# Kernel tuning notes

Measured on AMD Instinct MI355X. Metric: run time of the kernel, lower is better.

Reference implementation:

```python
import jax, jax.numpy as jnp
import numpy as np

T, B, I, H, O, L = 256, 128, 128, 512, 1, 5


def setup_inputs() -> dict:
    key = jax.random.key(0)
    ks = jax.random.split(key, 12)
    k = 1.0 / np.sqrt(H)
    u = lambda kk, shape: jax.random.uniform(kk, shape, jnp.float32, -k, k)
    inp = {
        "input_seq": jax.random.normal(ks[0], (T, B, I), jnp.float32),
        # layer 0: input size I, 2 directions
        "W_ih0": u(ks[1], (2, 3 * H, I)),
        "W_hh0": u(ks[2], (2, 3 * H, H)),
        "b_ih0": u(ks[3], (2, 3 * H)),
        "b_hh0": u(ks[4], (2, 3 * H)),
        # layers 1..4: input size 2H, 2 directions
        "W_ih": u(ks[5], (L - 1, 2, 3 * H, 2 * H)),
        "W_hh": u(ks[6], (L - 1, 2, 3 * H, H)),
        "b_ih": u(ks[7], (L - 1, 2, 3 * H)),
        "b_hh": u(ks[8], (L - 1, 2, 3 * H)),
        "fc_w": u(ks[9], (O, 2 * H)),
        "fc_b": u(ks[10], (O,)),
    }
    return inp


def _gru_dir(x, Wih, Whh, bih, bhh):
    # x: [T, B, in]; precompute input-side gates for all timesteps
    gx = jnp.einsum('tbi,gi->tbg', x, Wih) + bih  # [T, B, 3H]

    def step(h, g):
        gh = h @ Whh.T + bhh  # [B, 3H]
        xr, xz, xn = jnp.split(g, 3, axis=-1)
        hr, hz, hn = jnp.split(gh, 3, axis=-1)
        r = jax.nn.sigmoid(xr + hr)
        z = jax.nn.sigmoid(xz + hz)
        n = jnp.tanh(xn + r * hn)
        h_new = (1.0 - z) * n + z * h
        return h_new, h_new

    h0 = jnp.zeros((x.shape[1], Whh.shape[1]), x.dtype)
    _, hs = jax.lax.scan(step, h0, gx)
    return hs  # [T, B, H]


def _bigru_layer(x, Wih, Whh, bih, bhh):
    # Wih: [2, 3H, in]; direction 0 = forward, 1 = backward (PyTorch convention)
    fwd = _gru_dir(x, Wih[0], Whh[0], bih[0], bhh[0])
    bwd = _gru_dir(x[::-1], Wih[1], Whh[1], bih[1], bhh[1])[::-1]
    return jnp.concatenate([fwd, bwd], axis=-1)  # [T, B, 2H]


def reference(input_seq, W_ih0, W_hh0, b_ih0, b_hh0, W_ih, W_hh, b_ih, b_hh, fc_w, fc_b):
    # 5-layer bidirectional GRU (eval mode: inter-layer dropout inactive)
    h = _bigru_layer(input_seq, W_ih0, W_hh0, b_ih0, b_hh0)
    for l in range(L - 1):
        h = _bigru_layer(h, W_ih[l], W_hh[l], b_ih[l], b_hh[l])
    out = jnp.einsum('tbh,oh->tbo', h, fc_w) + fc_b
    return jax.nn.sigmoid(out)
```

## Files before the change

### kernel.cpp

```cpp
#include <hip/hip_runtime.h>
#include <hip/hip_bf16.h>

#define T_ 256
#define B_ 128
#define H_ 512
#define G3 1536
#define SCH 32
#define NCH 8
#define RWG 32
#define BGRP 8

typedef __attribute__((ext_vector_type(8))) short short8;
typedef __attribute__((ext_vector_type(4))) short short4v;
typedef __attribute__((ext_vector_type(4))) float f32x4;

static __device__ __forceinline__ float b2f(short s){
    unsigned u = ((unsigned)(unsigned short)s) << 16;
    return __builtin_bit_cast(float, u);
}
static __device__ __forceinline__ short f2b(float f){
    __hip_bfloat16 h = __float2bfloat16(f);
    return __builtin_bit_cast(short, h);
}
static __device__ __forceinline__ void gload16(const void* g, void* l){
    __builtin_amdgcn_global_load_lds(
        (__attribute__((address_space(1))) void*)(void*)g,
        (__attribute__((address_space(3))) void*)l, 16, 0, 0);
}
static __device__ __forceinline__ short8 gload_sc(const short* p){
    short8 v;
    asm volatile("global_load_dwordx4 %0, %1, off sc0 sc1"
                 : "=v"(v) : "v"(p) : "memory");
    return v;
}
static __device__ __forceinline__ void gstore_sc(short* p, short v){
    asm volatile("global_store_short %0, %1, off sc0 sc1"
                 :: "v"(p), "v"(v) : "memory");
}
static __device__ __forceinline__ void wait_vm0(){
    asm volatile("s_waitcnt vmcnt(0)" ::: "memory");
}

__global__ void cvt_f32_to_bf16(const float* __restrict__ src, short* __restrict__ dst, int n){
    int i = (blockIdx.x * blockDim.x + threadIdx.x) * 4;
    int stride = gridDim.x * blockDim.x * 4;
    for (; i + 3 < n; i += stride){
        float4 v = *(const float4*)(src + i);
        short4v o;
        o[0] = f2b(v.x); o[1] = f2b(v.y); o[2] = f2b(v.z); o[3] = f2b(v.w);
        *(short4v*)(dst + i) = o;
    }
}

__global__ __launch_bounds__(256) void gx_gemm(
    const short* __restrict__ A,
    const short* __restrict__ W,
    const float* __restrict__ bias,
    short* __restrict__ gxc,
    int K, int t0f, int t0b_lo)
{
    __shared__ __align__(16) short sA[4096];
    __shared__ __align__(16) short sB[4096];
    const int dir = blockIdx.z;
    const int t0 = dir ? t0b_lo : t0f;
    const int m0 = blockIdx.x * 128;
    const int n0 = blockIdx.y * 128;
    const short* Ae = A + (size_t)(t0 * B_) * K;
    const short* We = W + (size_t)dir * G3 * K;
    short* out = gxc + (size_t)dir * ((size_t)SCH * B_ * G3);

    const int tid = threadIdx.x, wv = tid >> 6, lane = tid & 63;
    const int moff = (wv & 1) * 64, noff = (wv >> 1) * 64;
    const int e0 = wv * 1024 + lane * 8, e1 = e0 + 512;
    const short* a0 = Ae + (size_t)(m0 + (e0 >> 5)) * K + (e0 & 31);
    const short* a1 = Ae + (size_t)(m0 + (e1 >> 5)) * K + (e1 & 31);
    const short* b0 = We + (size_t)(n0 + (e0 >> 5)) * K + (e0 & 31);
    const short* b1 = We + (size_t)(n0 + (e1 >> 5)) * K + (e1 & 31);
    short* sa0 = &sA[wv * 1024];  short* sa1 = &sA[wv * 1024 + 512];
    short* sb0 = &sB[wv * 1024];  short* sb1 = &sB[wv * 1024 + 512];

    f32x4 acc[4][4] = {};
    const int lr = lane & 15, lk = (lane >> 4) * 8;

    for (int kk = 0; kk < K; kk += 32){
        gload16(a0 + kk, sa0); gload16(a1 + kk, sa1);
        gload16(b0 + kk, sb0); gload16(b1 + kk, sb1);
        __syncthreads();
        short8 ar[4], br[4];
        #pragma unroll
        for (int i = 0; i < 4; ++i) ar[i] = *(const short8*)&sA[(moff + i*16 + lr) * 32 + lk];
        #pragma unroll
        for (int i = 0; i < 4; ++i) br[i] = *(const short8*)&sB[(noff + i*16 + lr) * 32 + lk];
        #pragma unroll
        for (int ai = 0; ai < 4; ++ai)
            #pragma unroll
            for (int bi = 0; bi < 4; ++bi)
                acc[ai][bi] = __builtin_amdgcn_mfma_f32_16x16x32_bf16(ar[ai], br[bi], acc[ai][bi], 0, 0, 0);
        __syncthreads();
    }

    #pragma unroll
    for (int ai = 0; ai < 4; ++ai){
        #pragma unroll
        for (int bi = 0; bi < 4; ++bi){
            int col = n0 + noff + bi*16 + lr;
            float bv = bias[dir * G3 + col];
            #pragma unroll
            for (int r = 0; r < 4; ++r){
                int row = m0 + moff + ai*16 + ((lane >> 4) << 2) + r;
                out[(size_t)row * G3 + col] = f2b(acc[ai][bi][r] + bv);
            }
        }
    }
}

__global__ __launch_bounds__(256, 1) void rec_kernel(
    const short* __restrict__ gxc,
    const short* __restrict__ Whh,
    const float* __restrict__ bhh,
    short* __restrict__ xout,
    float* __restrict__ hfm,
    short* __restrict__ hbb,
    int* __restrict__ bar,
    int t0f, int t0b_hi, int first, int base)
{
    __shared__ __align__(16) short lds_h[32 * 520];
    const int tid = threadIdx.x, wv = tid >> 6, lane = tid & 63;
    const int ug = blockIdx.x >> 2, bg = blockIdx.x & 3, dir = blockIdx.y;
    const int u0 = ug * 64 + wv * 16;
    const int m0 = bg * 32;
    const int lr = lane & 15, lk = (lane >> 4) * 8;
    const int crow = (lane >> 4) * 4;

    const short* Wd = Whh + (size_t)dir * G3 * H_;
    short8 wreg[3][16];
    #pragma unroll
    for (int g = 0; g < 3; ++g)
        #pragma unroll
        for (int kk = 0; kk < 16; ++kk)
            wreg[g][kk] = *(const short8*)&Wd[(size_t)(g*H_ + u0 + lr) * H_ + kk*32 + lk];

    float bh[3];
    #pragma unroll
    for (int g = 0; g < 3; ++g) bh[g] = bhh[dir*G3 + g*H_ + u0 + lr];

    float hreg[2][4];
    #pragma unroll
    for (int mt = 0; mt < 2; ++mt)
        #pragma unroll
        for (int r = 0; r < 4; ++r)
            hreg[mt][r] = first ? 0.f
                : hfm[((size_t)dir*B_ + m0 + mt*16 + crow + r)*H_ + u0 + lr];

    int* cnt = bar + (dir*4 + bg) * 32;
    const short* gxd = gxc + (size_t)dir * ((size_t)SCH * B_ * G3);

    const int srow = tid >> 3, scol0 = (tid & 7) * 8;

    float gv[3][2][4];
    {
        const int tl0 = dir ? (SCH - 1) : 0;
        const short* gb = gxd + ((size_t)(tl0 * B_) + m0 + crow) * G3 + u0 + lr;
        #pragma unroll
        for (int g = 0; g < 3; ++g)
            #pragma unroll
            for (int mt = 0; mt < 2; ++mt)
                #pragma unroll
                for (int r = 0; r < 4; ++r)
                    gv[g][mt][r] = b2f(gb[(size_t)(mt*16 + r) * G3 + g * H_]);
    }

    for (int sl = 0; sl < SCH; ++sl){
        const int t  = dir ? (t0b_hi - sl) : (t0f + sl);
        const int rp = sl & 1;

        {
            const short* hsrc = hbb + ((size_t)(rp*2 + dir) * B_ + m0) * H_;
            short8 hv[8];
            #pragma unroll
            for (int c = 0; c < 8; ++c)
                hv[c] = gload_sc(hsrc + (size_t)srow * H_ + scol0 + c*64);
            wait_vm0();
            #pragma unroll
            for (int c = 0; c < 8; ++c)
                *(short8*)&lds_h[srow * 520 + scol0 + c*64] = hv[c];
        }
        __syncthreads();

        f32x4 acc[3][2] = {};
        #pragma unroll
        for (int kk = 0; kk < 16; ++kk){
            short8 a0 = *(const short8*)&lds_h[(lr)      * 520 + kk*32 + lk];
            short8 a1 = *(const short8*)&lds_h[(16 + lr) * 520 + kk*32 + lk];
            #pragma unroll
            for (int g = 0; g < 3; ++g){
                acc[g][0] = __builtin_amdgcn_mfma_f32_16x16x32_bf16(a0, wreg[g][kk], acc[g][0], 0, 0, 0);
                acc[g][1] = __builtin_amdgcn_mfma_f32_16x16x32_bf16(a1, wreg[g][kk], acc[g][1], 0, 0, 0);
            }
        }

        short* hwr = hbb + ((size_t)((rp^1)*2 + dir) * B_) * H_;
        #pragma unroll
        for (int mt = 0; mt < 2; ++mt){
            #pragma unroll
            for (int r = 0; r < 4; ++r){
                float gr = acc[0][mt][r] + bh[0] + gv[0][mt][r];
                float gz = acc[1][mt][r] + bh[1] + gv[1][mt][r];
                float gn = acc[2][mt][r] + bh[2];
                float xn = gv[2][mt][r];
                float rg = 1.f / (1.f + __expf(-gr));
                float zg = 1.f / (1.f + __expf(-gz));
                float e2 = __expf(2.f * (xn + rg * gn));
                float ng = 1.f - 2.f / (e2 + 1.f);
                float hn = (1.f - zg) * ng + zg * hreg[mt][r];
                hreg[mt][r] = hn;
                short h16 = f2b(hn);
                const int row = m0 + mt*16 + crow + r;
                gstore_sc(hwr + (size_t)row * H_ + u0 + lr, h16);
                xout[((size_t)t * B_ + row) * 1024 + dir*H_ + u0 + lr] = h16;
            }
        }

        wait_vm0();
        __syncthreads();
        if (tid == 0)
            __hip_atomic_fetch_add(cnt, 1, __ATOMIC_RELAXED, __HIP_MEMORY_SCOPE_AGENT);

        if (sl + 1 < SCH){
            const int tln = dir ? (SCH - 2 - sl) : (sl + 1);
            const short* gb = gxd + ((size_t)(tln * B_) + m0 + crow) * G3 + u0 + lr;
            #pragma unroll
            for (int g = 0; g < 3; ++g)
                #pragma unroll
                for (int mt = 0; mt < 2; ++mt)
                    #pragma unroll
                    for (int r = 0; r < 4; ++r)
                        gv[g][mt][r] = b2f(gb[(size_t)(mt*16 + r) * G3 + g * H_]);
        }

        if (tid == 0){
            const int tgt = (base + sl + 1) * BGRP;
            while (__hip_atomic_load(cnt, __ATOMIC_RELAXED, __HIP_MEMORY_SCOPE_AGENT) < tgt)
                __builtin_amdgcn_s_sleep(1);
        }
        __syncthreads();
    }

    #pragma unroll
    for (int mt = 0; mt < 2; ++mt)
        #pragma unroll
        for (int r = 0; r < 4; ++r)
            hfm[((size_t)dir*B_ + m0 + mt*16 + crow + r)*H_ + u0 + lr] = hreg[mt][r];
}

__global__ void fc_kernel(const short* __restrict__ h, const float* __restrict__ w,
                          const float* __restrict__ b, float* __restrict__ out){
    int wid = threadIdx.x >> 6, lane = threadIdx.x & 63;
    int tb = blockIdx.x * 4 + wid;
    const short* hp = h + (size_t)tb * 1024 + lane * 16;
    float s = 0.f;
    #pragma unroll
    for (int c = 0; c < 2; ++c){
        short8 v = *(const short8*)(hp + c * 8);
        #pragma unroll
        for (int e = 0; e < 8; ++e) s += b2f(v[e]) * w[lane * 16 + c * 8 + e];
    }
    #pragma unroll
    for (int o = 32; o; o >>= 1) s += __shfl_down(s, o);
    if (lane == 0) out[tb] = 1.f / (1.f + __expf(-(s + b[0])));
}

extern "C" void kernel_launch(void* const* d_in, const int* in_sizes, int n_in,
                              void* d_out, int out_size, void* d_ws, size_t ws_size,
                              hipStream_t stream){
    const float* input_seq = (const float*)d_in[0];
    const float* W_ih0 = (const float*)d_in[1];
    const float* W_hh0 = (const float*)d_in[2];
    const float* b_ih0 = (const float*)d_in[3];
    const float* b_hh0 = (const float*)d_in[4];
    const float* W_ih  = (const float*)d_in[5];
    const float* W_hh  = (const float*)d_in[6];
    const float* b_ih  = (const float*)d_in[7];
    const float* b_hh  = (const float*)d_in[8];
    const float* fc_w  = (const float*)d_in[9];
    const float* fc_b  = (const float*)d_in[10];
    (void)in_sizes; (void)n_in; (void)out_size; (void)ws_size;

    char* ws = (char*)d_ws;
    size_t off = 0;
    auto alloc = [&](size_t bytes) -> char* {
        char* p = ws + off; off += (bytes + 255) & ~(size_t)255; return p;
    };
    short* actA = (short*)alloc((size_t)T_*B_*1024 * 2);
    short* actB = (short*)alloc((size_t)T_*B_*1024 * 2);
    short* gxc  = (short*)alloc((size_t)2*SCH*B_*G3 * 2);
    short* wihl = (short*)alloc((size_t)2*G3*1024 * 2);
    short* whhl = (short*)alloc((size_t)2*G3*H_ * 2);
    float* hfm  = (float*)alloc((size_t)2*B_*H_ * 4);
    short* hbb  = (short*)alloc((size_t)2*2*B_*H_ * 2);
    int*   bar  = (int*)alloc(4096);

    auto cvt = [&](const float* s, short* d, size_t n){
        int blocks = (int)((n/4 + 255) / 256); if (blocks > 4096) blocks = 4096;
        hipLaunchKernelGGL(cvt_f32_to_bf16, dim3(blocks), dim3(256), 0, stream, s, d, (int)n);
    };

    cvt(input_seq, actB, (size_t)T_*B_*128);

    for (int l = 0; l < 5; ++l){
        const int K = l ? 1024 : 128;
        cvt(l ? W_ih + (size_t)(l-1)*2*G3*1024 : W_ih0, wihl, (size_t)2*G3*K);
        cvt(l ? W_hh + (size_t)(l-1)*2*G3*H_   : W_hh0, whhl, (size_t)2*G3*H_);
        const short* IN  = (l & 1) ? actA : actB;
        short*       OUT = (l & 1) ? actB : actA;
        const float* bi = l ? b_ih + (size_t)(l-1)*2*G3 : b_ih0;
        const float* bh = l ? b_hh + (size_t)(l-1)*2*G3 : b_hh0;

        hipMemsetAsync(hbb, 0, (size_t)2*2*B_*H_*2, stream);
        hipMemsetAsync(bar, 0, 4096, stream);

        for (int q = 0; q < NCH; ++q){
            const int t0f    = SCH * q;
            const int t0b_hi = T_ - 1 - SCH * q;
            const int t0b_lo = t0b_hi - SCH + 1;
            hipLaunchKernelGGL(gx_gemm, dim3(SCH*B_/128, G3/128, 2), dim3(256), 0, stream,
                               IN, wihl, bi, gxc, K, t0f, t0b_lo);
            hipLaunchKernelGGL(rec_kernel, dim3(RWG, 2), dim3(256), 0, stream,
                               gxc, whhl, bh, OUT, hfm, hbb, bar, t0f, t0b_hi, q == 0, q*SCH);
        }
    }
    hipLaunchKernelGGL(fc_kernel, dim3((T_*B_)/4), dim3(256), 0, stream,
                       actA, fc_w, fc_b, (float*)d_out);
}
```

Measured before the change: 6.799 ms.

## Replace atomic counter barrier with per-block flags and coalesce hidden-state stores

The shared atomic counter barrier is replaced by per-workgroup step flags. Each block publishes its step with a plain store and polls its 8 peers' flags with two vector loads before it reads h. The wait moves to the start of each step, so the next gx prefetch overlaps with waiting. New hidden states are staged through LDS so that the hbb and xout writes become 16-byte coalesced stores instead of scattered 2-byte ones. This adds an extra LDS round-trip and __syncthreads per step, and relies on the flags being correctly initialised and on the ping-pong parity now being derived from the global step.

```diff
diff --git a/kernel.cpp b/kernel.cpp
--- a/kernel.cpp
+++ b/kernel.cpp
@@ -13,6 +13,7 @@
 typedef __attribute__((ext_vector_type(8))) short short8;
 typedef __attribute__((ext_vector_type(4))) short short4v;
 typedef __attribute__((ext_vector_type(4))) float f32x4;
+typedef __attribute__((ext_vector_type(4))) unsigned int uint4v;
 
 static __device__ __forceinline__ float b2f(short s){
     unsigned u = ((unsigned)(unsigned short)s) << 16;
@@ -26,6 +27,9 @@
     __builtin_amdgcn_global_load_lds(
         (__attribute__((address_space(1))) void*)(void*)g,
         (__attribute__((address_space(3))) void*)l, 16, 0, 0);
+}
+static __device__ __forceinline__ void wait_vm0(){
+    asm volatile("s_waitcnt vmcnt(0)" ::: "memory");
 }
 static __device__ __forceinline__ short8 gload_sc(const short* p){
     short8 v;
@@ -33,12 +37,22 @@
                  : "=v"(v) : "v"(p) : "memory");
     return v;
 }
-static __device__ __forceinline__ void gstore_sc(short* p, short v){
-    asm volatile("global_store_short %0, %1, off sc0 sc1"
+static __device__ __forceinline__ void gstore16_sc(short* p, short8 v){
+    asm volatile("global_store_dwordx4 %0, %1, off sc0 sc1"
                  :: "v"(p), "v"(v) : "memory");
 }
-static __device__ __forceinline__ void wait_vm0(){
-    asm volatile("s_waitcnt vmcnt(0)" ::: "memory");
+static __device__ __forceinline__ void store_flag(unsigned int* p, unsigned int v){
+    asm volatile("global_store_dword %0, %1, off sc0 sc1"
+                 :: "v"(p), "v"(v) : "memory");
+}
+static __device__ __forceinline__ void load_flags8(const unsigned int* p, unsigned int* f){
+    uint4v a, b;
+    asm volatile("global_load_dwordx4 %0, %2, off sc0 sc1\n\t"
+                 "global_load_dwordx4 %1, %3, off sc0 sc1\n\t"
+                 "s_waitcnt vmcnt(0)"
+                 : "=v"(a), "=v"(b) : "v"(p), "v"(p + 4) : "memory");
+    f[0]=a.x; f[1]=a.y; f[2]=a.z; f[3]=a.w;
+    f[4]=b.x; f[5]=b.y; f[6]=b.z; f[7]=b.w;
 }
 
 __global__ void cvt_f32_to_bf16(const float* __restrict__ src, short* __restrict__ dst, int n){
@@ -121,16 +135,19 @@
     short* __restrict__ xout,
     float* __restrict__ hfm,
     short* __restrict__ hbb,
-    int* __restrict__ bar,
+    unsigned int* __restrict__ flags,
     int t0f, int t0b_hi, int first, int base)
 {
     __shared__ __align__(16) short lds_h[32 * 520];
+    __shared__ __align__(16) short lds_out[32 * 72];
     const int tid = threadIdx.x, wv = tid >> 6, lane = tid & 63;
     const int ug = blockIdx.x >> 2, bg = blockIdx.x & 3, dir = blockIdx.y;
-    const int u0 = ug * 64 + wv * 16;
+    const int u0w = ug * 64;
+    const int u0 = u0w + wv * 16;
     const int m0 = bg * 32;
     const int lr = lane & 15, lk = (lane >> 4) * 8;
     const int crow = (lane >> 4) * 4;
+    const int srow = tid >> 3, scol0 = (tid & 7) * 8;
 
     const short* Wd = Whh + (size_t)dir * G3 * H_;
     short8 wreg[3][16];
@@ -152,10 +169,8 @@
             hreg[mt][r] = first ? 0.f
                 : hfm[((size_t)dir*B_ + m0 + mt*16 + crow + r)*H_ + u0 + lr];
 
-    int* cnt = bar + (dir*4 + bg) * 32;
+    unsigned int* flg = flags + (dir*4 + bg) * 32;
     const short* gxd = gxc + (size_t)dir * ((size_t)SCH * B_ * G3);
-
-    const int srow = tid >> 3, scol0 = (tid & 7) * 8;
 
     float gv[3][2][4];
     {
@@ -171,8 +186,22 @@
     }
 
     for (int sl = 0; sl < SCH; ++sl){
+        const int sg = base + sl;
         const int t  = dir ? (t0b_hi - sl) : (t0f + sl);
-        const int rp = sl & 1;
+        const int rp = sg & 1;
+
+        if (tid == 0){
+            unsigned int f[8];
+            for (;;){
+                load_flags8(flg, f);
+                bool ok = true;
+                #pragma unroll
+                for (int j = 0; j < 8; ++j) ok &= (f[j] >= (unsigned int)sg);
+                if (ok) break;
+                __builtin_amdgcn_s_sleep(1);
+            }
+        }
+        __syncthreads();
 
         {
             const short* hsrc = hbb + ((size_t)(rp*2 + dir) * B_ + m0) * H_;
@@ -199,7 +228,6 @@
             }
         }
 
-        short* hwr = hbb + ((size_t)((rp^1)*2 + dir) * B_) * H_;
         #pragma unroll
         for (int mt = 0; mt < 2; ++mt){
             #pragma unroll
@@ -214,17 +242,21 @@
                 float ng = 1.f - 2.f / (e2 + 1.f);
                 float hn = (1.f - zg) * ng + zg * hreg[mt][r];
                 hreg[mt][r] = hn;
-                short h16 = f2b(hn);
-                const int row = m0 + mt*16 + crow + r;
-                gstore_sc(hwr + (size_t)row * H_ + u0 + lr, h16);
-                xout[((size_t)t * B_ + row) * 1024 + dir*H_ + u0 + lr] = h16;
+                lds_out[(mt*16 + crow + r) * 72 + wv*16 + lr] = f2b(hn);
             }
         }
+        __syncthreads();
+
+        {
+            short8 ov = *(const short8*)&lds_out[srow * 72 + scol0];
+            short* hwr = hbb + ((size_t)((rp^1)*2 + dir) * B_ + m0 + srow) * H_ + u0w + scol0;
+            gstore16_sc(hwr, ov);
+            *(short8*)&xout[((size_t)t * B_ + m0 + srow) * 1024 + dir*H_ + u0w + scol0] = ov;
+        }
 
         wait_vm0();
         __syncthreads();
-        if (tid == 0)
-            __hip_atomic_fetch_add(cnt, 1, __ATOMIC_RELAXED, __HIP_MEMORY_SCOPE_AGENT);
+        if (tid == 0) store_flag(&flg[ug], (unsigned int)(sg + 1));
 
         if (sl + 1 < SCH){
             const int tln = dir ? (SCH - 2 - sl) : (sl + 1);
@@ -237,13 +269,6 @@
                     for (int r = 0; r < 4; ++r)
                         gv[g][mt][r] = b2f(gb[(size_t)(mt*16 + r) * G3 + g * H_]);
         }
-
-        if (tid == 0){
-            const int tgt = (base + sl + 1) * BGRP;
-            while (__hip_atomic_load(cnt, __ATOMIC_RELAXED, __HIP_MEMORY_SCOPE_AGENT) < tgt)
-                __builtin_amdgcn_s_sleep(1);
-        }
-        __syncthreads();
     }
 
     #pragma unroll
@@ -298,7 +323,7 @@
     short* whhl = (short*)alloc((size_t)2*G3*H_ * 2);
     float* hfm  = (float*)alloc((size_t)2*B_*H_ * 4);
     short* hbb  = (short*)alloc((size_t)2*2*B_*H_ * 2);
-    int*   bar  = (int*)alloc(4096);
+    unsigned int* bar = (unsigned int*)alloc(4096);
 
     auto cvt = [&](const float* s, short* d, size_t n){
         int blocks = (int)((n/4 + 255) / 256); if (blocks > 4096) blocks = 4096;
```

Result: faster. 6.539 ms (-3.8%).
